# Kernel optimization log

Hardware: AMD Instinct MI355X
Metric: run time of the kernel (lower is better)

## Reference

```python
import jax, jax.numpy as jnp
import numpy as np

N_NODES = 100000
N_EDGES = 3200000
F_IN = 256
HEADS = 8
C_OUT = 8
NEG_SLOPE = 0.2


def setup_inputs() -> dict:
    key = jax.random.key(0)
    k1, k2, k3, k4, k5, k6 = jax.random.split(key, 6)
    x = jax.random.normal(k1, (N_NODES, F_IN), dtype=jnp.float32)
    edge_index = jax.random.randint(k2, (2, N_EDGES), 0, N_NODES, dtype=jnp.int64)
    W = jax.random.normal(k3, (F_IN, HEADS * C_OUT), dtype=jnp.float32) * (1.0 / np.sqrt(F_IN))
    att_src = jax.random.normal(k4, (HEADS, C_OUT), dtype=jnp.float32) * 0.1
    att_dst = jax.random.normal(k5, (HEADS, C_OUT), dtype=jnp.float32) * 0.1
    bias = jax.random.normal(k6, (HEADS * C_OUT,), dtype=jnp.float32) * 0.01
    return {"x": x, "edge_index": edge_index, "W": W, "att_src": att_src, "att_dst": att_dst, "bias": bias}


def reference(x, edge_index, W, att_src, att_dst, bias):
    # GATConv (PyG semantics), concat=True, inference (dropout off).
    N = x.shape[0]
    H, C = att_src.shape
    h = (x @ W).reshape(N, H, C)                      # [N,H,C] transformed features
    a_src = jnp.einsum('nhc,hc->nh', h, att_src)      # [N,H]
    a_dst = jnp.einsum('nhc,hc->nh', h, att_dst)      # [N,H]
    src, dst = edge_index[0], edge_index[1]
    # per-edge raw attention logits
    e = jax.nn.leaky_relu(a_src[src] + a_dst[dst], NEG_SLOPE)  # [E,H]
    # segment softmax over incoming edges of each destination node
    m = jax.ops.segment_max(e, dst, num_segments=N)            # [N,H]
    e = jnp.exp(e - m[dst])
    s = jax.ops.segment_sum(e, dst, num_segments=N)            # [N,H]
    alpha = e / (s[dst] + 1e-16)                               # [E,H]
    # scatter-add weighted neighbor features
    out = jax.ops.segment_sum(alpha[:, :, None] * h[src], dst, num_segments=N)  # [N,H,C]
    return out.reshape(N, H * C) + bias
```

## Files before the change

### kernel.cpp

```cpp
#include <hip/hip_runtime.h>
#include <hip/hip_fp16.h>
#include <math.h>

#define F_IN 256
#define HC 64
#define NHEAD 8
#define NEG 0.2f
#define BSH 7
#define BSZ 128
#define CAP 5376
#define HCAP 2944

typedef __attribute__((ext_vector_type(8))) short bf16x8;
typedef __attribute__((ext_vector_type(4))) float f32x4;

union BV { uint4 q; bf16x8 v; };

__device__ __forceinline__ unsigned int hi_pair(float a, float b) {
  return __builtin_amdgcn_perm(__float_as_uint(a), __float_as_uint(b), 0x03020706u);
}
__device__ __forceinline__ unsigned int lo_pair(float a, float b) {
  float ra = a - __uint_as_float(__float_as_uint(a) & 0xffff0000u);
  float rb = b - __uint_as_float(__float_as_uint(b) & 0xffff0000u);
  return __builtin_amdgcn_perm(__float_as_uint(ra), __float_as_uint(rb), 0x03020706u);
}

__global__ __launch_bounds__(256) void k_prep(const float* __restrict__ W,
                                              unsigned short* __restrict__ Wp,
                                              int* __restrict__ bcursor, int NB) {
  int b = blockIdx.x, t = threadIdx.x;
  if (b >= 64) {
    int i = (b - 64) * 256 + t;
    if (i < NB) bcursor[i] = 0;
    return;
  }
  int idx = b * 256 + t;
  int k = idx >> 6, c = idx & 63;
  float w = W[idx];
  unsigned int u = __float_as_uint(w);
  unsigned short hi = (unsigned short)((u + 0x7fffu + ((u >> 16) & 1u)) >> 16);
  float r = w - __uint_as_float((unsigned int)hi << 16);
  unsigned int ur = __float_as_uint(r);
  unsigned short lo = (unsigned short)((ur + 0x7fffu + ((ur >> 16) & 1u)) >> 16);
  int ks = k >> 5, j = k & 7, lg = (k >> 3) & 3;
  int lane = lg * 16 + (c & 15), cg = c >> 4;
  int off = ((ks * 4 + cg) * 64 + lane) * 8 + j;
  Wp[off] = hi;
  Wp[16384 + off] = lo;
}

__global__ __launch_bounds__(256, 3) void k_gemm(
    const float* __restrict__ x, const uint4* __restrict__ Wp4,
    const float* __restrict__ att_src, const float* __restrict__ att_dst,
    __half2* __restrict__ h2, float* __restrict__ asrc, float* __restrict__ adst, int N) {
  int t = threadIdx.x;
  int wv = t >> 6, l = t & 63;
  int lr = l & 15, lg = l >> 4;
  int r0 = blockIdx.x * 128 + wv * 32;
  int ra = r0 + lr;      if (ra > N - 1) ra = N - 1;
  int rb = r0 + 16 + lr; if (rb > N - 1) rb = N - 1;
  const float* xr0 = x + (size_t)ra * F_IN + lg * 8;
  const float* xr1 = x + (size_t)rb * F_IN + lg * 8;
  const uint4* wp = Wp4 + l;

  float as4[4], ad4[4];
#pragma unroll
  for (int cg = 0; cg < 4; cg++) {
    as4[cg] = att_src[cg * 16 + lr];
    ad4[cg] = att_dst[cg * 16 + lr];
  }

  f32x4 acc[2][4];
#pragma unroll
  for (int i = 0; i < 2; i++)
#pragma unroll
    for (int j = 0; j < 4; j++) acc[i][j] = (f32x4){0.f, 0.f, 0.f, 0.f};

#pragma unroll
  for (int ks = 0; ks < 8; ks++) {
    float4 p0 = *(const float4*)(xr0 + ks * 32);
    float4 q0 = *(const float4*)(xr0 + ks * 32 + 4);
    float4 p1 = *(const float4*)(xr1 + ks * 32);
    float4 q1 = *(const float4*)(xr1 + ks * 32 + 4);
    BV bh[4], bl[4];
#pragma unroll
    for (int cg = 0; cg < 4; cg++) {
      bh[cg].q = wp[(ks * 4 + cg) * 64];
      bl[cg].q = wp[2048 + (ks * 4 + cg) * 64];
    }
    BV ah0, al0, ah1, al1;
    ah0.q.x = hi_pair(p0.x, p0.y); ah0.q.y = hi_pair(p0.z, p0.w);
    ah0.q.z = hi_pair(q0.x, q0.y); ah0.q.w = hi_pair(q0.z, q0.w);
    al0.q.x = lo_pair(p0.x, p0.y); al0.q.y = lo_pair(p0.z, p0.w);
    al0.q.z = lo_pair(q0.x, q0.y); al0.q.w = lo_pair(q0.z, q0.w);
    ah1.q.x = hi_pair(p1.x, p1.y); ah1.q.y = hi_pair(p1.z, p1.w);
    ah1.q.z = hi_pair(q1.x, q1.y); ah1.q.w = hi_pair(q1.z, q1.w);
    al1.q.x = lo_pair(p1.x, p1.y); al1.q.y = lo_pair(p1.z, p1.w);
    al1.q.z = lo_pair(q1.x, q1.y); al1.q.w = lo_pair(q1.z, q1.w);
#pragma unroll
    for (int cg = 0; cg < 4; cg++) {
      acc[0][cg] = __builtin_amdgcn_mfma_f32_16x16x32_bf16(ah0.v, bh[cg].v, acc[0][cg], 0, 0, 0);
      acc[0][cg] = __builtin_amdgcn_mfma_f32_16x16x32_bf16(al0.v, bh[cg].v, acc[0][cg], 0, 0, 0);
      acc[0][cg] = __builtin_amdgcn_mfma_f32_16x16x32_bf16(ah0.v, bl[cg].v, acc[0][cg], 0, 0, 0);
      acc[1][cg] = __builtin_amdgcn_mfma_f32_16x16x32_bf16(ah1.v, bh[cg].v, acc[1][cg], 0, 0, 0);
      acc[1][cg] = __builtin_amdgcn_mfma_f32_16x16x32_bf16(al1.v, bh[cg].v, acc[1][cg], 0, 0, 0);
      acc[1][cg] = __builtin_amdgcn_mfma_f32_16x16x32_bf16(ah1.v, bl[cg].v, acc[1][cg], 0, 0, 0);
    }
  }

#pragma unroll
  for (int rg = 0; rg < 2; rg++) {
#pragma unroll
    for (int tt = 0; tt < 4; tt++) {
      int node = r0 + rg * 16 + 4 * lg + tt;
      bool ok = node < N;
      float v0 = acc[rg][0][tt], v1 = acc[rg][1][tt], v2 = acc[rg][2][tt], v3 = acc[rg][3][tt];
      float o0 = __shfl_xor(v0, 1), o1 = __shfl_xor(v1, 1);
      float o2 = __shfl_xor(v2, 1), o3 = __shfl_xor(v3, 1);
      if (ok && !(l & 1)) {
        size_t hb = (size_t)node * 32 + (lr >> 1);
        h2[hb]      = __halves2half2(__float2half_rn(v0), __float2half_rn(o0));
        h2[hb + 8]  = __halves2half2(__float2half_rn(v1), __float2half_rn(o1));
        h2[hb + 16] = __halves2half2(__float2half_rn(v2), __float2half_rn(o2));
        h2[hb + 24] = __halves2half2(__float2half_rn(v3), __float2half_rn(o3));
      }
#pragma unroll
      for (int cg = 0; cg < 4; cg++) {
        float v = (cg == 0) ? v0 : (cg == 1) ? v1 : (cg == 2) ? v2 : v3;
        float s = v * as4[cg];
        float d = v * ad4[cg];
        s += __shfl_xor(s, 1); d += __shfl_xor(d, 1);
        s += __shfl_xor(s, 2); d += __shfl_xor(d, 2);
        s += __shfl_xor(s, 4); d += __shfl_xor(d, 4);
        if (ok && !(l & 7)) {
          int hd = 2 * cg + (lr >> 3);
          asrc[node * NHEAD + hd] = s;
          adst[node * NHEAD + hd] = d;
        }
      }
    }
  }
}

__global__ __launch_bounds__(512) void k_partition(
    const int* __restrict__ edge, int* __restrict__ bcursor,
    unsigned int* __restrict__ entries, int E, int NB) {
  __shared__ unsigned long long srt8[8192];
  __shared__ int hist[1024];
  __shared__ int loff[1024];
  __shared__ int basearr[1024];
  __shared__ int pr[512];
  int t = threadIdx.x;
  int base = blockIdx.x * 8192;
  int cblk = min(8192, E - base);
  for (int i = t; i < 1024; i += 512) hist[i] = 0;
  __syncthreads();
#pragma unroll
  for (int j = 0; j < 16; j++) {
    int e = base + j * 512 + t;
    if (e < E) atomicAdd(&hist[edge[E + e] >> BSH], 1);
  }
  __syncthreads();
  int a = hist[2 * t], b = hist[2 * t + 1];
  pr[t] = a + b;
  __syncthreads();
  for (int off = 1; off < 512; off <<= 1) {
    int add = (t >= off) ? pr[t - off] : 0;
    __syncthreads();
    pr[t] += add;
    __syncthreads();
  }
  int excl = pr[t] - (a + b);
  loff[2 * t] = excl;
  loff[2 * t + 1] = excl + a;
  if (a > 0 && 2 * t < NB) basearr[2 * t] = atomicAdd(&bcursor[2 * t], a);
  if (b > 0 && 2 * t + 1 < NB) basearr[2 * t + 1] = atomicAdd(&bcursor[2 * t + 1], b);
  hist[2 * t] = excl;
  hist[2 * t + 1] = excl + a;
  __syncthreads();
#pragma unroll
  for (int j = 0; j < 16; j++) {
    int e = base + j * 512 + t;
    if (e < E) {
      int s = edge[e], d = edge[E + e];
      int p = atomicAdd(&hist[d >> BSH], 1);
      srt8[p] = ((unsigned long long)(unsigned int)d << 32) | (unsigned int)s;
    }
  }
  __syncthreads();
  for (int i = t; i < cblk; i += 512) {
    unsigned long long v = srt8[i];
    int d = (int)(v >> 32), s = (int)(v & 0xFFFFFFFFu);
    int bk = d >> BSH;
    int local = basearr[bk] + (i - loff[bk]);
    if (local < CAP)
      entries[(size_t)bk * CAP + local] = ((unsigned int)(d & (BSZ - 1)) << 17) | (unsigned int)s;
  }
}

__global__ __launch_bounds__(512, 6) void k_bagg(
    const unsigned int* __restrict__ entries, const int* __restrict__ bcursor,
    const __half2* __restrict__ h2, const float* __restrict__ asrc,
    const float* __restrict__ adst, const float* __restrict__ bias,
    float* __restrict__ out, int N) {
  __shared__ int srt[HCAP];
  __shared__ int hist[64];
  __shared__ int cur[64];
  __shared__ int off[65];
  __shared__ int tmp[64];
  int t = threadIdx.x;
  int bkt = blockIdx.x >> 1;
  int hf = blockIdx.x & 1;
  int n0 = (bkt << BSH) + (hf << 6);
  int ncnt = min(64, N - n0);
  if (ncnt <= 0) return;
  int cnt = bcursor[bkt];
  if (cnt > CAP) cnt = CAP;
  const unsigned int* ebase = entries + (size_t)bkt * CAP;
  if (t < 64) hist[t] = 0;
  __syncthreads();
  for (int i = t; i < cnt; i += 512) {
    int d = (int)(ebase[i] >> 17);
    if ((d >> 6) == hf) atomicAdd(&hist[d & 63], 1);
  }
  __syncthreads();
  if (t < 64) tmp[t] = hist[t];
  __syncthreads();
  for (int o = 1; o < 64; o <<= 1) {
    int add = (t < 64 && t >= o) ? tmp[t - o] : 0;
    __syncthreads();
    if (t < 64) tmp[t] += add;
    __syncthreads();
  }
  if (t < 64) { off[t] = tmp[t] - hist[t]; cur[t] = tmp[t] - hist[t]; }
  if (t == 63) off[64] = tmp[63];
  __syncthreads();
  for (int i = t; i < cnt; i += 512) {
    unsigned int v = ebase[i];
    int d = (int)(v >> 17);
    if ((d >> 6) == hf) {
      int p = atomicAdd(&cur[d & 63], 1);
      if (p < HCAP) srt[p] = (int)(v & 0x1FFFF);
    }
  }
  __syncthreads();
  int wv = t >> 6, l = t & 63;
  int eslot = l >> 3, cg = l & 7;
  for (int nd = wv; nd < ncnt; nd += 8) {
    int node = n0 + nd;
    int sbeg = min(off[nd], HCAP), send = min(off[nd + 1], HCAP);
    float ad = adst[node * NHEAD + cg];
    float a0 = 0.f, a1 = 0.f, a2 = 0.f, a3 = 0.f;
    float a4 = 0.f, a5 = 0.f, a6 = 0.f, a7 = 0.f;
    float wsum = 0.f;
    for (int k = sbeg; k < send; k += 8) {
      int idx = k + eslot;
      bool val = idx < send;
      int s = srt[val ? idx : send - 1];
      float lg = asrc[s * NHEAD + cg] + ad;
      float w = __expf(fmaxf(lg, NEG * lg));
      w = val ? w : 0.f;
      union { uint4 q; __half2 h[4]; } u;
      u.q = *((const uint4*)(h2 + (size_t)s * 32) + cg);
      float2 f0 = __half22float2(u.h[0]);
      float2 f1 = __half22float2(u.h[1]);
      float2 f2 = __half22float2(u.h[2]);
      float2 f3 = __half22float2(u.h[3]);
      a0 = fmaf(w, f0.x, a0); a1 = fmaf(w, f0.y, a1);
      a2 = fmaf(w, f1.x, a2); a3 = fmaf(w, f1.y, a3);
      a4 = fmaf(w, f2.x, a4); a5 = fmaf(w, f2.y, a5);
      a6 = fmaf(w, f3.x, a6); a7 = fmaf(w, f3.y, a7);
      wsum += w;
    }
#pragma unroll
    for (int m = 8; m < 64; m <<= 1) {
      a0 += __shfl_xor(a0, m); a1 += __shfl_xor(a1, m);
      a2 += __shfl_xor(a2, m); a3 += __shfl_xor(a3, m);
      a4 += __shfl_xor(a4, m); a5 += __shfl_xor(a5, m);
      a6 += __shfl_xor(a6, m); a7 += __shfl_xor(a7, m);
      wsum += __shfl_xor(wsum, m);
    }
    if (l < 8) {
      float inv = wsum > 0.f ? 1.0f / wsum : 0.f;
      float4 b0 = *(const float4*)&bias[cg * 8];
      float4 b1 = *(const float4*)&bias[cg * 8 + 4];
      float4 r0, r1;
      r0.x = fmaf(a0, inv, b0.x); r0.y = fmaf(a1, inv, b0.y);
      r0.z = fmaf(a2, inv, b0.z); r0.w = fmaf(a3, inv, b0.w);
      r1.x = fmaf(a4, inv, b1.x); r1.y = fmaf(a5, inv, b1.y);
      r1.z = fmaf(a6, inv, b1.z); r1.w = fmaf(a7, inv, b1.w);
      *(float4*)&out[(size_t)node * HC + cg * 8] = r0;
      *(float4*)&out[(size_t)node * HC + cg * 8 + 4] = r1;
    }
  }
}

extern "C" void kernel_launch(void* const* d_in, const int* in_sizes, int n_in,
                              void* d_out, int out_size, void* d_ws, size_t ws_size,
                              hipStream_t stream) {
  const float* x = (const float*)d_in[0];
  const int* edge = (const int*)d_in[1];
  const float* W = (const float*)d_in[2];
  const float* att_src = (const float*)d_in[3];
  const float* att_dst = (const float*)d_in[4];
  const float* bias = (const float*)d_in[5];
  int N = in_sizes[0] / F_IN;
  int E = in_sizes[1] / 2;
  float* out = (float*)d_out;
  int NB = (N + BSZ - 1) >> BSH;

  unsigned short* Wp = (unsigned short*)d_ws;
  __half2* h2 = (__half2*)((char*)d_ws + 65536);
  float* asrc = (float*)(h2 + (size_t)N * 32);
  float* adst = asrc + (size_t)N * NHEAD;
  int* bcursor = (int*)(adst + (size_t)N * NHEAD);
  unsigned int* entries = (unsigned int*)(bcursor + ((NB + 3) & ~3));

  int nch = (E + 8191) / 8192;
  int nzb = (NB + 255) / 256;

  k_prep<<<64 + nzb, 256, 0, stream>>>(W, Wp, bcursor, NB);
  k_gemm<<<(N + 127) / 128, 256, 0, stream>>>(x, (const uint4*)Wp, att_src, att_dst, h2, asrc, adst, N);
  k_partition<<<nch, 512, 0, stream>>>(edge, bcursor, entries, E, NB);
  k_bagg<<<2 * NB, 512, 0, stream>>>(entries, bcursor, h2, asrc, adst, bias, out, N);
}
```

Measured before the change: 324.8 us.

## Fuse GEMM and edge-partition kernels into one interleaved heterogeneous launch

```diff
diff --git a/kernel.cpp b/kernel.cpp
--- a/kernel.cpp
+++ b/kernel.cpp
@@ -49,109 +49,115 @@
   Wp[16384 + off] = lo;
 }
 
-__global__ __launch_bounds__(256, 3) void k_gemm(
+__global__ __launch_bounds__(512, 4) void k_fused(
     const float* __restrict__ x, const uint4* __restrict__ Wp4,
     const float* __restrict__ att_src, const float* __restrict__ att_dst,
-    __half2* __restrict__ h2, float* __restrict__ asrc, float* __restrict__ adst, int N) {
-  int t = threadIdx.x;
-  int wv = t >> 6, l = t & 63;
-  int lr = l & 15, lg = l >> 4;
-  int r0 = blockIdx.x * 128 + wv * 32;
-  int ra = r0 + lr;      if (ra > N - 1) ra = N - 1;
-  int rb = r0 + 16 + lr; if (rb > N - 1) rb = N - 1;
-  const float* xr0 = x + (size_t)ra * F_IN + lg * 8;
-  const float* xr1 = x + (size_t)rb * F_IN + lg * 8;
-  const uint4* wp = Wp4 + l;
-
-  float as4[4], ad4[4];
-#pragma unroll
-  for (int cg = 0; cg < 4; cg++) {
-    as4[cg] = att_src[cg * 16 + lr];
-    ad4[cg] = att_dst[cg * 16 + lr];
-  }
-
-  f32x4 acc[2][4];
-#pragma unroll
-  for (int i = 0; i < 2; i++)
-#pragma unroll
-    for (int j = 0; j < 4; j++) acc[i][j] = (f32x4){0.f, 0.f, 0.f, 0.f};
-
-#pragma unroll
-  for (int ks = 0; ks < 8; ks++) {
-    float4 p0 = *(const float4*)(xr0 + ks * 32);
-    float4 q0 = *(const float4*)(xr0 + ks * 32 + 4);
-    float4 p1 = *(const float4*)(xr1 + ks * 32);
-    float4 q1 = *(const float4*)(xr1 + ks * 32 + 4);
-    BV bh[4], bl[4];
-#pragma unroll
-    for (int cg = 0; cg < 4; cg++) {
-      bh[cg].q = wp[(ks * 4 + cg) * 64];
-      bl[cg].q = wp[2048 + (ks * 4 + cg) * 64];
-    }
-    BV ah0, al0, ah1, al1;
-    ah0.q.x = hi_pair(p0.x, p0.y); ah0.q.y = hi_pair(p0.z, p0.w);
-    ah0.q.z = hi_pair(q0.x, q0.y); ah0.q.w = hi_pair(q0.z, q0.w);
-    al0.q.x = lo_pair(p0.x, p0.y); al0.q.y = lo_pair(p0.z, p0.w);
-    al0.q.z = lo_pair(q0.x, q0.y); al0.q.w = lo_pair(q0.z, q0.w);
-    ah1.q.x = hi_pair(p1.x, p1.y); ah1.q.y = hi_pair(p1.z, p1.w);
-    ah1.q.z = hi_pair(q1.x, q1.y); ah1.q.w = hi_pair(q1.z, q1.w);
-    al1.q.x = lo_pair(p1.x, p1.y); al1.q.y = lo_pair(p1.z, p1.w);
-    al1.q.z = lo_pair(q1.x, q1.y); al1.q.w = lo_pair(q1.z, q1.w);
-#pragma unroll
-    for (int cg = 0; cg < 4; cg++) {
-      acc[0][cg] = __builtin_amdgcn_mfma_f32_16x16x32_bf16(ah0.v, bh[cg].v, acc[0][cg], 0, 0, 0);
-      acc[0][cg] = __builtin_amdgcn_mfma_f32_16x16x32_bf16(al0.v, bh[cg].v, acc[0][cg], 0, 0, 0);
-      acc[0][cg] = __builtin_amdgcn_mfma_f32_16x16x32_bf16(ah0.v, bl[cg].v, acc[0][cg], 0, 0, 0);
-      acc[1][cg] = __builtin_amdgcn_mfma_f32_16x16x32_bf16(ah1.v, bh[cg].v, acc[1][cg], 0, 0, 0);
-      acc[1][cg] = __builtin_amdgcn_mfma_f32_16x16x32_bf16(al1.v, bh[cg].v, acc[1][cg], 0, 0, 0);
-      acc[1][cg] = __builtin_amdgcn_mfma_f32_16x16x32_bf16(ah1.v, bl[cg].v, acc[1][cg], 0, 0, 0);
-    }
-  }
-
-#pragma unroll
-  for (int rg = 0; rg < 2; rg++) {
-#pragma unroll
-    for (int tt = 0; tt < 4; tt++) {
-      int node = r0 + rg * 16 + 4 * lg + tt;
-      bool ok = node < N;
-      float v0 = acc[rg][0][tt], v1 = acc[rg][1][tt], v2 = acc[rg][2][tt], v3 = acc[rg][3][tt];
-      float o0 = __shfl_xor(v0, 1), o1 = __shfl_xor(v1, 1);
-      float o2 = __shfl_xor(v2, 1), o3 = __shfl_xor(v3, 1);
-      if (ok && !(l & 1)) {
-        size_t hb = (size_t)node * 32 + (lr >> 1);
-        h2[hb]      = __halves2half2(__float2half_rn(v0), __float2half_rn(o0));
-        h2[hb + 8]  = __halves2half2(__float2half_rn(v1), __float2half_rn(o1));
-        h2[hb + 16] = __halves2half2(__float2half_rn(v2), __float2half_rn(o2));
-        h2[hb + 24] = __halves2half2(__float2half_rn(v3), __float2half_rn(o3));
-      }
-#pragma unroll
-      for (int cg = 0; cg < 4; cg++) {
-        float v = (cg == 0) ? v0 : (cg == 1) ? v1 : (cg == 2) ? v2 : v3;
-        float s = v * as4[cg];
-        float d = v * ad4[cg];
-        s += __shfl_xor(s, 1); d += __shfl_xor(d, 1);
-        s += __shfl_xor(s, 2); d += __shfl_xor(d, 2);
-        s += __shfl_xor(s, 4); d += __shfl_xor(d, 4);
-        if (ok && !(l & 7)) {
-          int hd = 2 * cg + (lr >> 3);
-          asrc[node * NHEAD + hd] = s;
-          adst[node * NHEAD + hd] = d;
-        }
-      }
-    }
-  }
-}
-
-__global__ __launch_bounds__(512) void k_partition(
+    __half2* __restrict__ h2, float* __restrict__ asrc, float* __restrict__ adst,
     const int* __restrict__ edge, int* __restrict__ bcursor,
-    unsigned int* __restrict__ entries, int E, int NB) {
+    unsigned int* __restrict__ entries, int N, int E, int NB, int NG, int NP) {
   __shared__ unsigned long long srt8[8192];
   __shared__ int hist[1024];
   __shared__ int loff[1024];
   __shared__ int basearr[1024];
   __shared__ int pr[512];
+  int b = blockIdx.x;
+  int mn = min(NG, NP), m2 = 2 * mn;
+  int type, idx;
+  if (b < m2) { type = b & 1; idx = b >> 1; }
+  else { type = (NG > NP) ? 0 : 1; idx = mn + (b - m2); }
   int t = threadIdx.x;
-  int base = blockIdx.x * 8192;
+
+  if (type == 0) {
+    int wv = t >> 6, l = t & 63;
+    int lr = l & 15, lg = l >> 4;
+    int r0 = idx * 256 + wv * 32;
+    int ra = r0 + lr;      if (ra > N - 1) ra = N - 1;
+    int rb = r0 + 16 + lr; if (rb > N - 1) rb = N - 1;
+    const float* xr0 = x + (size_t)ra * F_IN + lg * 8;
+    const float* xr1 = x + (size_t)rb * F_IN + lg * 8;
+    const uint4* wp = Wp4 + l;
+
+    float as4[4], ad4[4];
+#pragma unroll
+    for (int cg = 0; cg < 4; cg++) {
+      as4[cg] = att_src[cg * 16 + lr];
+      ad4[cg] = att_dst[cg * 16 + lr];
+    }
+
+    f32x4 acc[2][4];
+#pragma unroll
+    for (int i = 0; i < 2; i++)
+#pragma unroll
+      for (int j = 0; j < 4; j++) acc[i][j] = (f32x4){0.f, 0.f, 0.f, 0.f};
+
+#pragma unroll
+    for (int ks = 0; ks < 8; ks++) {
+      float4 p0 = *(const float4*)(xr0 + ks * 32);
+      float4 q0 = *(const float4*)(xr0 + ks * 32 + 4);
+      float4 p1 = *(const float4*)(xr1 + ks * 32);
+      float4 q1 = *(const float4*)(xr1 + ks * 32 + 4);
+      BV bh[4], bl[4];
+#pragma unroll
+      for (int cg = 0; cg < 4; cg++) {
+        bh[cg].q = wp[(ks * 4 + cg) * 64];
+        bl[cg].q = wp[2048 + (ks * 4 + cg) * 64];
+      }
+      BV ah0, al0, ah1, al1;
+      ah0.q.x = hi_pair(p0.x, p0.y); ah0.q.y = hi_pair(p0.z, p0.w);
+      ah0.q.z = hi_pair(q0.x, q0.y); ah0.q.w = hi_pair(q0.z, q0.w);
+      al0.q.x = lo_pair(p0.x, p0.y); al0.q.y = lo_pair(p0.z, p0.w);
+      al0.q.z = lo_pair(q0.x, q0.y); al0.q.w = lo_pair(q0.z, q0.w);
+      ah1.q.x = hi_pair(p1.x, p1.y); ah1.q.y = hi_pair(p1.z, p1.w);
+      ah1.q.z = hi_pair(q1.x, q1.y); ah1.q.w = hi_pair(q1.z, q1.w);
+      al1.q.x = lo_pair(p1.x, p1.y); al1.q.y = lo_pair(p1.z, p1.w);
+      al1.q.z = lo_pair(q1.x, q1.y); al1.q.w = lo_pair(q1.z, q1.w);
+#pragma unroll
+      for (int cg = 0; cg < 4; cg++) {
+        acc[0][cg] = __builtin_amdgcn_mfma_f32_16x16x32_bf16(ah0.v, bh[cg].v, acc[0][cg], 0, 0, 0);
+        acc[0][cg] = __builtin_amdgcn_mfma_f32_16x16x32_bf16(al0.v, bh[cg].v, acc[0][cg], 0, 0, 0);
+        acc[0][cg] = __builtin_amdgcn_mfma_f32_16x16x32_bf16(ah0.v, bl[cg].v, acc[0][cg], 0, 0, 0);
+        acc[1][cg] = __builtin_amdgcn_mfma_f32_16x16x32_bf16(ah1.v, bh[cg].v, acc[1][cg], 0, 0, 0);
+        acc[1][cg] = __builtin_amdgcn_mfma_f32_16x16x32_bf16(al1.v, bh[cg].v, acc[1][cg], 0, 0, 0);
+        acc[1][cg] = __builtin_amdgcn_mfma_f32_16x16x32_bf16(ah1.v, bl[cg].v, acc[1][cg], 0, 0, 0);
+      }
+    }
+
+#pragma unroll
+    for (int rg = 0; rg < 2; rg++) {
+#pragma unroll
+      for (int tt = 0; tt < 4; tt++) {
+        int node = r0 + rg * 16 + 4 * lg + tt;
+        bool ok = node < N;
+        float v0 = acc[rg][0][tt], v1 = acc[rg][1][tt], v2 = acc[rg][2][tt], v3 = acc[rg][3][tt];
+        float o0 = __shfl_xor(v0, 1), o1 = __shfl_xor(v1, 1);
+        float o2 = __shfl_xor(v2, 1), o3 = __shfl_xor(v3, 1);
+        if (ok && !(l & 1)) {
+          size_t hb = (size_t)node * 32 + (lr >> 1);
+          h2[hb]      = __halves2half2(__float2half_rn(v0), __float2half_rn(o0));
+          h2[hb + 8]  = __halves2half2(__float2half_rn(v1), __float2half_rn(o1));
+          h2[hb + 16] = __halves2half2(__float2half_rn(v2), __float2half_rn(o2));
+          h2[hb + 24] = __halves2half2(__float2half_rn(v3), __float2half_rn(o3));
+        }
+#pragma unroll
+        for (int cg = 0; cg < 4; cg++) {
+          float v = (cg == 0) ? v0 : (cg == 1) ? v1 : (cg == 2) ? v2 : v3;
+          float s = v * as4[cg];
+          float d = v * ad4[cg];
+          s += __shfl_xor(s, 1); d += __shfl_xor(d, 1);
+          s += __shfl_xor(s, 2); d += __shfl_xor(d, 2);
+          s += __shfl_xor(s, 4); d += __shfl_xor(d, 4);
+          if (ok && !(l & 7)) {
+            int hd = 2 * cg + (lr >> 3);
+            asrc[node * NHEAD + hd] = s;
+            adst[node * NHEAD + hd] = d;
+          }
+        }
+      }
+    }
+    return;
+  }
+
+  int base = idx * 8192;
   int cblk = min(8192, E - base);
   for (int i = t; i < 1024; i += 512) hist[i] = 0;
   __syncthreads();
@@ -161,8 +167,8 @@
     if (e < E) atomicAdd(&hist[edge[E + e] >> BSH], 1);
   }
   __syncthreads();
-  int a = hist[2 * t], b = hist[2 * t + 1];
-  pr[t] = a + b;
+  int a = hist[2 * t], bb = hist[2 * t + 1];
+  pr[t] = a + bb;
   __syncthreads();
   for (int off = 1; off < 512; off <<= 1) {
     int add = (t >= off) ? pr[t - off] : 0;
@@ -170,11 +176,11 @@
     pr[t] += add;
     __syncthreads();
   }
-  int excl = pr[t] - (a + b);
+  int excl = pr[t] - (a + bb);
   loff[2 * t] = excl;
   loff[2 * t + 1] = excl + a;
   if (a > 0 && 2 * t < NB) basearr[2 * t] = atomicAdd(&bcursor[2 * t], a);
-  if (b > 0 && 2 * t + 1 < NB) basearr[2 * t + 1] = atomicAdd(&bcursor[2 * t + 1], b);
+  if (bb > 0 && 2 * t + 1 < NB) basearr[2 * t + 1] = atomicAdd(&bcursor[2 * t + 1], bb);
   hist[2 * t] = excl;
   hist[2 * t + 1] = excl + a;
   __syncthreads();
@@ -316,11 +322,13 @@
   int* bcursor = (int*)(adst + (size_t)N * NHEAD);
   unsigned int* entries = (unsigned int*)(bcursor + ((NB + 3) & ~3));
 
-  int nch = (E + 8191) / 8192;
+  int NG = (N + 255) / 256;
+  int NP = (E + 8191) / 8192;
   int nzb = (NB + 255) / 256;
 
   k_prep<<<64 + nzb, 256, 0, stream>>>(W, Wp, bcursor, NB);
-  k_gemm<<<(N + 127) / 128, 256, 0, stream>>>(x, (const uint4*)Wp, att_src, att_dst, h2, asrc, adst, N);
-  k_partition<<<nch, 512, 0, stream>>>(edge, bcursor, entries, E, NB);
+  k_fused<<<NG + NP, 512, 0, stream>>>(x, (const uint4*)Wp, att_src, att_dst,
+                                       h2, asrc, adst, edge, bcursor, entries,
+                                       N, E, NB, NG, NP);
   k_bagg<<<2 * NB, 512, 0, stream>>>(entries, bcursor, h2, asrc, adst, bias, out, N);
 }
```

After: 322.7 us. About the same (-0.6%).

## Stage x tiles through double-buffered LDS with async global_load_lds in GEMM

Applied to the files above, without the earlier changes.

```diff
diff --git a/kernel.cpp b/kernel.cpp
--- a/kernel.cpp
+++ b/kernel.cpp
@@ -49,19 +49,16 @@
   Wp[16384 + off] = lo;
 }
 
-__global__ __launch_bounds__(256, 3) void k_gemm(
+__global__ __launch_bounds__(512, 4) void k_gemm(
     const float* __restrict__ x, const uint4* __restrict__ Wp4,
     const float* __restrict__ att_src, const float* __restrict__ att_dst,
-    __half2* __restrict__ h2, float* __restrict__ asrc, float* __restrict__ adst, int N) {
+    __half2* __restrict__ h2, float* __restrict__ asrc, float* __restrict__ adst,
+    int N) {
+  __shared__ __align__(16) char xb[65536];
   int t = threadIdx.x;
   int wv = t >> 6, l = t & 63;
   int lr = l & 15, lg = l >> 4;
-  int r0 = blockIdx.x * 128 + wv * 32;
-  int ra = r0 + lr;      if (ra > N - 1) ra = N - 1;
-  int rb = r0 + 16 + lr; if (rb > N - 1) rb = N - 1;
-  const float* xr0 = x + (size_t)ra * F_IN + lg * 8;
-  const float* xr1 = x + (size_t)rb * F_IN + lg * 8;
-  const uint4* wp = Wp4 + l;
+  int r0blk = blockIdx.x * 256;
 
   float as4[4], ad4[4];
 #pragma unroll
@@ -69,6 +66,7 @@
     as4[cg] = att_src[cg * 16 + lr];
     ad4[cg] = att_dst[cg * 16 + lr];
   }
+  const uint4* wp = Wp4 + l;
 
   f32x4 acc[2][4];
 #pragma unroll
@@ -76,12 +74,37 @@
 #pragma unroll
     for (int j = 0; j < 4; j++) acc[i][j] = (f32x4){0.f, 0.f, 0.f, 0.f};
 
+#define STAGE(ks_, buf_)                                                        \
+  {                                                                             \
+    _Pragma("unroll")                                                           \
+    for (int rd = 0; rd < 4; rd++) {                                            \
+      int Lbase = rd * 512 + wv * 64;                                           \
+      int L = Lbase + l;                                                        \
+      int r_ = L >> 3;                                                          \
+      int g_ = (L & 7) ^ (r_ & 7);                                              \
+      int grow = r0blk + r_; if (grow > N - 1) grow = N - 1;                    \
+      __builtin_amdgcn_global_load_lds(                                         \
+          (const void*)(x + (size_t)grow * F_IN + (ks_) * 32 + g_ * 4),         \
+          (void*)(xb + (buf_) * 32768 + (size_t)Lbase * 16), 16, 0, 0);         \
+    }                                                                           \
+  }
+
+  STAGE(0, 0);
+  __syncthreads();
+  int ra_t = wv * 32 + lr, rb_t = ra_t + 16;
+  int s0 = ra_t * 8 + ((lg * 2 + 0) ^ (ra_t & 7));
+  int s1 = ra_t * 8 + ((lg * 2 + 1) ^ (ra_t & 7));
+  int s2 = rb_t * 8 + ((lg * 2 + 0) ^ (rb_t & 7));
+  int s3 = rb_t * 8 + ((lg * 2 + 1) ^ (rb_t & 7));
+
 #pragma unroll
   for (int ks = 0; ks < 8; ks++) {
-    float4 p0 = *(const float4*)(xr0 + ks * 32);
-    float4 q0 = *(const float4*)(xr0 + ks * 32 + 4);
-    float4 p1 = *(const float4*)(xr1 + ks * 32);
-    float4 q1 = *(const float4*)(xr1 + ks * 32 + 4);
+    if (ks < 7) STAGE(ks + 1, (ks + 1) & 1);
+    const char* cb = xb + (ks & 1) * 32768;
+    float4 p0 = *(const float4*)(cb + (size_t)s0 * 16);
+    float4 q0 = *(const float4*)(cb + (size_t)s1 * 16);
+    float4 p1 = *(const float4*)(cb + (size_t)s2 * 16);
+    float4 q1 = *(const float4*)(cb + (size_t)s3 * 16);
     BV bh[4], bl[4];
 #pragma unroll
     for (int cg = 0; cg < 4; cg++) {
@@ -106,8 +129,11 @@
       acc[1][cg] = __builtin_amdgcn_mfma_f32_16x16x32_bf16(al1.v, bh[cg].v, acc[1][cg], 0, 0, 0);
       acc[1][cg] = __builtin_amdgcn_mfma_f32_16x16x32_bf16(ah1.v, bl[cg].v, acc[1][cg], 0, 0, 0);
     }
-  }
-
+    __syncthreads();
+  }
+#undef STAGE
+
+  int r0 = r0blk + wv * 32;
 #pragma unroll
   for (int rg = 0; rg < 2; rg++) {
 #pragma unroll
@@ -316,11 +342,12 @@
   int* bcursor = (int*)(adst + (size_t)N * NHEAD);
   unsigned int* entries = (unsigned int*)(bcursor + ((NB + 3) & ~3));
 
-  int nch = (E + 8191) / 8192;
+  int NG = (N + 255) / 256;
+  int NP = (E + 8191) / 8192;
   int nzb = (NB + 255) / 256;
 
   k_prep<<<64 + nzb, 256, 0, stream>>>(W, Wp, bcursor, NB);
-  k_gemm<<<(N + 127) / 128, 256, 0, stream>>>(x, (const uint4*)Wp, att_src, att_dst, h2, asrc, adst, N);
-  k_partition<<<nch, 512, 0, stream>>>(edge, bcursor, entries, E, NB);
+  k_gemm<<<NG, 512, 0, stream>>>(x, (const uint4*)Wp, att_src, att_dst, h2, asrc, adst, N);
+  k_partition<<<NP, 512, 0, stream>>>(edge, bcursor, entries, E, NB);
   k_bagg<<<2 * NB, 512, 0, stream>>>(entries, bcursor, h2, asrc, adst, bias, out, N);
 }
```

Measured after the change: 322.2 us. About the same (-0.8%).
